# Kernel tuning notes

Hardware: AMD Instinct MI355X
Metric: run time of the kernel (lower is better)

The kernel has to match this reference:

```python
import jax, jax.numpy as jnp
import numpy as np

N = 100000      # nodes
IN = 64         # in_channels
HID = 64        # hidden_channels
H2 = HID // 2   # per-sign channels
E = 1600000     # edges per sign


def _mean_aggr(x_src, edge_index, num_nodes):
    """Mean of x_src[src] scattered onto dst (PyG mean aggregation)."""
    src, dst = edge_index[0], edge_index[1]
    s = jax.ops.segment_sum(x_src[src], dst, num_segments=num_nodes)
    cnt = jax.ops.segment_sum(jnp.ones((src.shape[0],), x_src.dtype), dst,
                              num_segments=num_nodes)
    return s / jnp.maximum(cnt, 1.0)[:, None]


def setup_inputs() -> dict:
    key = jax.random.key(0)
    ks = jax.random.split(key, 12)
    x = jax.random.normal(ks[0], (N, IN), jnp.float32)
    pos_edge_index = jax.random.randint(ks[1], (2, E), 0, N)
    neg_edge_index = jax.random.randint(ks[2], (2, E), 0, N)

    def w(k, fan_in, fan_out):
        b = 1.0 / np.sqrt(fan_in)
        return jax.random.uniform(k, (fan_in, fan_out), jnp.float32, -b, b)

    return dict(
        x=x, pos_edge_index=pos_edge_index, neg_edge_index=neg_edge_index,
        # conv1 (first_aggr=True): lin_l (no bias applied via l), lin_r (bias)
        w1_pl=w(ks[3], IN, H2), w1_pr=w(ks[4], IN, H2), b1_p=jnp.zeros((H2,), jnp.float32),
        w1_nl=w(ks[5], IN, H2), w1_nr=w(ks[6], IN, H2), b1_n=jnp.zeros((H2,), jnp.float32),
        # conv2 (first_aggr=False): lin_l over cat of two aggregations (2*H2), lin_r over H2
        w2_pl=w(ks[7], 2 * H2, H2), w2_pr=w(ks[8], H2, H2), b2_p=jnp.zeros((H2,), jnp.float32),
        w2_nl=w(ks[9], 2 * H2, H2), w2_nr=w(ks[10], H2, H2), b2_n=jnp.zeros((H2,), jnp.float32),
    )


def reference(x, pos_edge_index, neg_edge_index,
              w1_pl, w1_pr, b1_p, w1_nl, w1_nr, b1_n,
              w2_pl, w2_pr, b2_p, w2_nl, w2_nr, b2_n):
    n = x.shape[0]
    # --- conv1, first_aggr=True ---
    agg_p = _mean_aggr(x, pos_edge_index, n)          # [N, IN]
    agg_n = _mean_aggr(x, neg_edge_index, n)
    out_pos = agg_p @ w1_pl + x @ w1_pr + b1_p         # [N, H2]
    out_neg = agg_n @ w1_nl + x @ w1_nr + b1_n
    z = jax.nn.relu(jnp.concatenate([out_pos, out_neg], axis=-1))  # [N, HID]

    # --- conv2, first_aggr=False ---
    h2 = z.shape[-1] // 2
    zp, zn = z[:, :h2], z[:, h2:]
    p1 = _mean_aggr(zp, pos_edge_index, n)
    p2 = _mean_aggr(zn, neg_edge_index, n)
    out_pos = jnp.concatenate([p1, p2], axis=-1) @ w2_pl + zp @ w2_pr + b2_p
    n1 = _mean_aggr(zn, pos_edge_index, n)
    n2 = _mean_aggr(zp, neg_edge_index, n)
    out_neg = jnp.concatenate([n1, n2], axis=-1) @ w2_nl + zn @ w2_nr + b2_n
    z = jax.nn.relu(jnp.concatenate([out_pos, out_neg], axis=-1))  # [N, HID]
    return z
```

## Files before the change

kernel.cpp:

```cpp
#include <hip/hip_runtime.h>
#include <hip/hip_fp16.h>

using uint = unsigned int;

static constexpr int NN  = 100000;
static constexpr int NE  = 1600000;
static constexpr int DIM = 64;
static constexpr int HH  = 32;
static constexpr int NBLK = (NN + 255) / 256;
static constexpr int HB   = 256;
static constexpr int CHUNK = NE / HB;
static constexpr int BSH  = 9;
static constexpr int BSZ  = 512;
static constexpr int NBKT = (NN + BSZ - 1) / BSZ;

__device__ __forceinline__ float2 up16(uint v) {
  __half2 h = *reinterpret_cast<__half2*>(&v);
  return __half22float2(h);
}
__device__ __forceinline__ uint pk16(float a, float b) {
  __half2 h = __floats2half2_rn(a, b);
  return *reinterpret_cast<uint*>(&h);
}


__global__ void c_hist(const int* __restrict__ pe, const int* __restrict__ ne,
                       int* __restrict__ part_hist) {
  const int set = blockIdx.y;
  const int* dstA = (set ? ne : pe) + NE;
  __shared__ int h[256];
  h[threadIdx.x] = 0;
  __syncthreads();
  int lo = blockIdx.x * CHUNK;
  int hi = lo + CHUNK;
  for (int i = lo + threadIdx.x; i < hi; i += 256)
    atomicAdd(&h[dstA[i] >> BSH], 1);
  __syncthreads();
  part_hist[(set * HB + blockIdx.x) * 256 + threadIdx.x] = h[threadIdx.x];
}

__global__ void c_colscan(int* __restrict__ part_hist, int* __restrict__ tot) {
  const int set = blockIdx.y;
  const int k   = blockIdx.x;
  const int t   = threadIdx.x;
  int v = part_hist[(set * HB + t) * 256 + k];
  __shared__ int sm[256];
  sm[t] = v;
  __syncthreads();
  for (int off = 1; off < 256; off <<= 1) {
    int add = (t >= off) ? sm[t - off] : 0;
    __syncthreads();
    sm[t] += add;
    __syncthreads();
  }
  part_hist[(set * HB + t) * 256 + k] = (t == 0) ? 0 : sm[t - 1];
  if (t == 255) tot[set * 256 + k] = sm[255];
}

__global__ void c_basescan(const int* __restrict__ tot, int* __restrict__ base) {
  const int t   = threadIdx.x;
  const int seg = t >> 8;
  const int idx = t & 255;
  int v = tot[seg * 256 + idx];
  __shared__ int sm[512];
  sm[t] = v;
  __syncthreads();
  for (int off = 1; off < 256; off <<= 1) {
    int add = (idx >= off) ? sm[t - off] : 0;
    __syncthreads();
    sm[t] += add;
    __syncthreads();
  }
  base[seg * 257 + idx] = (idx == 0) ? 0 : sm[t - 1];
  if (idx == 255) base[seg * 257 + 256] = sm[t];
}

__global__ void c_scatter(const int* __restrict__ pe, const int* __restrict__ ne,
                          const int* __restrict__ part_hist, const int* __restrict__ base,
                          uint* __restrict__ partP, uint* __restrict__ partN) {
  const int set = blockIdx.y;
  const int* srcA = set ? ne : pe;
  const int* dstA = srcA + NE;
  uint* part = set ? partN : partP;
  __shared__ int off[256];
  off[threadIdx.x] = base[set * 257 + threadIdx.x] +
                     part_hist[(set * HB + blockIdx.x) * 256 + threadIdx.x];
  __syncthreads();
  int lo = blockIdx.x * CHUNK;
  int hi = lo + CHUNK;
  for (int i = lo + threadIdx.x; i < hi; i += 256) {
    int src = srcA[i];
    int dst = dstA[i];
    int pos = atomicAdd(&off[dst >> BSH], 1);
    part[pos] = ((uint)src << BSH) | (uint)(dst & (BSZ - 1));
  }
}

__global__ void c_bucket(const uint* __restrict__ partP, const uint* __restrict__ partN,
                         const int* __restrict__ base,
                         int* __restrict__ row_p, int* __restrict__ row_n,
                         int* __restrict__ col_p, int* __restrict__ col_n,
                         const float* __restrict__ x,
                         const float* __restrict__ w1_pl, const float* __restrict__ w1_pr,
                         const float* __restrict__ b1_p,
                         const float* __restrict__ w1_nl, const float* __restrict__ w1_nr,
                         const float* __restrict__ b1_n,
                         uint* __restrict__ y1u, float* __restrict__ r1) {
  const int bx = blockIdx.x;
  const int t  = threadIdx.x;

  if (bx < 2 * NBKT) {
    const int set = bx / NBKT;
    const int k   = bx - set * NBKT;
    const uint* part = set ? partN : partP;
    int* row = set ? row_n : row_p;
    int* col = set ? col_n : col_p;
    const int lo = k * BSZ;
    const int hi = min(lo + BSZ, NN);
    const int s = base[set * 257 + k];
    const int e = base[set * 257 + k + 1];

    __shared__ int cnt[BSZ], rowl[BSZ], cnt2[BSZ];
    cnt[t] = 0; cnt[t + 256] = 0;
    cnt2[t] = 0; cnt2[t + 256] = 0;
    __syncthreads();
    for (int i = s + t; i < e; i += 256)
      atomicAdd(&cnt[part[i] & (BSZ - 1)], 1);
    __syncthreads();
    rowl[t] = cnt[t]; rowl[t + 256] = cnt[t + 256];
    __syncthreads();
    for (int off = 1; off < BSZ; off <<= 1) {
      int a0 = (t >= off) ? rowl[t - off] : 0;
      int a1 = (t + 256 >= off) ? rowl[t + 256 - off] : 0;
      __syncthreads();
      rowl[t] += a0; rowl[t + 256] += a1;
      __syncthreads();
    }
    if (lo + t < hi)        row[lo + t]        = s + (t ? rowl[t - 1] : 0);
    if (lo + t + 256 < hi)  row[lo + t + 256]  = s + rowl[t + 255];
    if (k == NBKT - 1 && t == 0) row[NN] = NE;
    for (int i = s + t; i < e; i += 256) {
      uint p = part[i];
      int l = p & (BSZ - 1);
      int pos = s + (l ? rowl[l - 1] : 0) + atomicAdd(&cnt2[l], 1);
      col[pos] = (int)(p >> BSH);
    }
    return;
  }

  const int pb   = bx - 2 * NBKT;
  const int h    = (pb >= NBLK) ? 1 : 0;
  const int nblk = pb - (h ? NBLK : 0);
  const float* wl   = h ? w1_nl : w1_pl;
  const float* wr   = h ? w1_nr : w1_pr;
  const float* bias = h ? b1_n  : b1_p;

  __shared__ float s_wl[DIM][HH];
  __shared__ float s_wr[DIM][HH];
  for (int i = t; i < DIM * HH; i += 256) {
    s_wl[i >> 5][i & 31] = wl[i];
    s_wr[i >> 5][i & 31] = wr[i];
  }
  __syncthreads();

  int node = nblk * 256 + t;
  if (node >= NN) return;

  float ay[HH], ar[HH];
#pragma unroll
  for (int j = 0; j < HH; ++j) { ay[j] = 0.f; ar[j] = bias[j]; }

  const float4* xrow = (const float4*)(x + (size_t)node * DIM);
#pragma unroll 4
  for (int k4 = 0; k4 < DIM / 4; ++k4) {
    float4 xv = xrow[k4];
#pragma unroll
    for (int u = 0; u < 4; ++u) {
      int k = k4 * 4 + u;
      float xk = (&xv.x)[u];
#pragma unroll
      for (int j = 0; j < HH; ++j) {
        ay[j] += xk * s_wl[k][j];
        ar[j] += xk * s_wr[k][j];
      }
    }
  }

  uint*  yo = y1u + (size_t)node * 32 + h * 16;
  float* ro = r1  + (size_t)node * 64 + h * 32;
#pragma unroll
  for (int j = 0; j < 16; ++j) yo[j] = pk16(ay[2 * j], ay[2 * j + 1]);
#pragma unroll
  for (int j = 0; j < HH; ++j) ro[j] = ar[j];
}

__global__ void k_aggr1(const uint* __restrict__ y1u,
                        const int* __restrict__ rp, const int* __restrict__ cp,
                        const int* __restrict__ rn, const int* __restrict__ cn,
                        const float* r1,
                        float* z) {
  int gid  = blockIdx.x * 256 + threadIdx.x;
  int node = gid >> 6;
  if (node >= NN) return;
  int lane = threadIdx.x & 63;
  int g = lane >> 2;
  int f = lane & 3;

  int s = rp[node], e = rp[node + 1];
  float a[8];
#pragma unroll
  for (int j = 0; j < 8; ++j) a[j] = 0.f;
  for (int i = s + g; i < e; i += 16) {
    int c = cp[i];
    uint4 v = *(const uint4*)&y1u[(size_t)c * 32 + 4 * f];
    float2 p0 = up16(v.x), p1 = up16(v.y), p2 = up16(v.z), p3 = up16(v.w);
    a[0] += p0.x; a[1] += p0.y; a[2] += p1.x; a[3] += p1.y;
    a[4] += p2.x; a[5] += p2.y; a[6] += p3.x; a[7] += p3.y;
  }
#pragma unroll
  for (int w = 4; w <= 32; w <<= 1) {
#pragma unroll
    for (int j = 0; j < 8; ++j) a[j] += __shfl_xor(a[j], w);
  }
  float invp = 1.f / (float)max(e - s, 1);

  s = rn[node]; e = rn[node + 1];
  float b[8];
#pragma unroll
  for (int j = 0; j < 8; ++j) b[j] = 0.f;
  for (int i = s + g; i < e; i += 16) {
    int c = cn[i];
    uint4 v = *(const uint4*)&y1u[(size_t)c * 32 + 16 + 4 * f];
    float2 p0 = up16(v.x), p1 = up16(v.y), p2 = up16(v.z), p3 = up16(v.w);
    b[0] += p0.x; b[1] += p0.y; b[2] += p1.x; b[3] += p1.y;
    b[4] += p2.x; b[5] += p2.y; b[6] += p3.x; b[7] += p3.y;
  }
#pragma unroll
  for (int w = 4; w <= 32; w <<= 1) {
#pragma unroll
    for (int j = 0; j < 8; ++j) b[j] += __shfl_xor(b[j], w);
  }
  float invn = 1.f / (float)max(e - s, 1);

  size_t base = (size_t)node * 64;
  if (g == 0) {
    const float4 r0 = *(const float4*)(r1 + base + 8 * f);
    const float4 r1v = *(const float4*)(r1 + base + 8 * f + 4);
    float4 o0, o1;
    o0.x = fmaxf(a[0] * invp + r0.x, 0.f);
    o0.y = fmaxf(a[1] * invp + r0.y, 0.f);
    o0.z = fmaxf(a[2] * invp + r0.z, 0.f);
    o0.w = fmaxf(a[3] * invp + r0.w, 0.f);
    o1.x = fmaxf(a[4] * invp + r1v.x, 0.f);
    o1.y = fmaxf(a[5] * invp + r1v.y, 0.f);
    o1.z = fmaxf(a[6] * invp + r1v.z, 0.f);
    o1.w = fmaxf(a[7] * invp + r1v.w, 0.f);
    *(float4*)(z + base + 8 * f) = o0;
    *(float4*)(z + base + 8 * f + 4) = o1;
  } else if (g == 1) {
    const float4 r0 = *(const float4*)(r1 + base + 32 + 8 * f);
    const float4 r1v = *(const float4*)(r1 + base + 32 + 8 * f + 4);
    float4 o0, o1;
    o0.x = fmaxf(b[0] * invn + r0.x, 0.f);
    o0.y = fmaxf(b[1] * invn + r0.y, 0.f);
    o0.z = fmaxf(b[2] * invn + r0.z, 0.f);
    o0.w = fmaxf(b[3] * invn + r0.w, 0.f);
    o1.x = fmaxf(b[4] * invn + r1v.x, 0.f);
    o1.y = fmaxf(b[5] * invn + r1v.y, 0.f);
    o1.z = fmaxf(b[6] * invn + r1v.z, 0.f);
    o1.w = fmaxf(b[7] * invn + r1v.w, 0.f);
    *(float4*)(z + base + 32 + 8 * f) = o0;
    *(float4*)(z + base + 32 + 8 * f + 4) = o1;
  }
}

__global__ void k_mid(const float* __restrict__ z,
                      const float* __restrict__ w2_pl, const float* __restrict__ w2_pr,
                      const float* __restrict__ b2_p,
                      const float* __restrict__ w2_nl, const float* __restrict__ w2_nr,
                      const float* __restrict__ b2_n,
                      uint* __restrict__ u_pos, uint* __restrict__ u_neg,
                      float* __restrict__ r2) {
  const int t = blockIdx.y;
  const float* mat;
  const float* bias = nullptr;
  int srcHalf;
  switch (t) {
    case 0: mat = w2_pl;            srcHalf = 0; break;
    case 1: mat = w2_nl;            srcHalf = 1; break;
    case 2: mat = w2_pl + 32 * 32;  srcHalf = 1; break;
    case 3: mat = w2_nl + 32 * 32;  srcHalf = 0; break;
    case 4: mat = w2_pr; bias = b2_p; srcHalf = 0; break;
    default: mat = w2_nr; bias = b2_n; srcHalf = 1; break;
  }

  __shared__ float s_m[HH][HH];
  for (int i = threadIdx.x; i < HH * HH; i += 256) s_m[i >> 5][i & 31] = mat[i];
  __syncthreads();

  int node = blockIdx.x * 256 + threadIdx.x;
  if (node >= NN) return;

  float acc[HH];
#pragma unroll
  for (int j = 0; j < HH; ++j) acc[j] = bias ? bias[j] : 0.f;

  const float4* zrow = (const float4*)(z + (size_t)node * 64 + srcHalf * 32);
#pragma unroll 4
  for (int k4 = 0; k4 < HH / 4; ++k4) {
    float4 v = zrow[k4];
#pragma unroll
    for (int u = 0; u < 4; ++u) {
      int k = k4 * 4 + u;
      float vv = (&v.x)[u];
#pragma unroll
      for (int j = 0; j < HH; ++j) acc[j] += vv * s_m[k][j];
    }
  }

  if (t < 4) {
    uint* o = (t < 2 ? u_pos : u_neg) + (size_t)node * 32 + (t & 1) * 16;
#pragma unroll
    for (int j = 0; j < 16; ++j) o[j] = pk16(acc[2 * j], acc[2 * j + 1]);
  } else {
    float* o = r2 + (size_t)node * 64 + (t - 4) * 32;
#pragma unroll
    for (int j = 0; j < HH; ++j) o[j] = acc[j];
  }
}

__global__ void k_aggr2(const uint* __restrict__ u_pos, const uint* __restrict__ u_neg,
                        const int* __restrict__ rp, const int* __restrict__ cp,
                        const int* __restrict__ rn, const int* __restrict__ cn,
                        const float* __restrict__ r2,
                        float* __restrict__ out) {
  int gid  = blockIdx.x * 256 + threadIdx.x;
  int node = gid >> 6;
  if (node >= NN) return;
  int lane = threadIdx.x & 63;
  int g = lane >> 3;
  int f = lane & 7;

  int s = rp[node], e = rp[node + 1];
  float a[8];
#pragma unroll
  for (int j = 0; j < 8; ++j) a[j] = 0.f;
  for (int i = s + g; i < e; i += 8) {
    int c = cp[i];
    uint4 v = *(const uint4*)&u_pos[(size_t)c * 32 + 4 * f];
    float2 p0 = up16(v.x), p1 = up16(v.y), p2 = up16(v.z), p3 = up16(v.w);
    a[0] += p0.x; a[1] += p0.y; a[2] += p1.x; a[3] += p1.y;
    a[4] += p2.x; a[5] += p2.y; a[6] += p3.x; a[7] += p3.y;
  }
#pragma unroll
  for (int w = 8; w <= 32; w <<= 1) {
#pragma unroll
    for (int j = 0; j < 8; ++j) a[j] += __shfl_xor(a[j], w);
  }
  float invp = 1.f / (float)max(e - s, 1);

  s = rn[node]; e = rn[node + 1];
  float b[8];
#pragma unroll
  for (int j = 0; j < 8; ++j) b[j] = 0.f;
  for (int i = s + g; i < e; i += 8) {
    int c = cn[i];
    uint4 v = *(const uint4*)&u_neg[(size_t)c * 32 + 4 * f];
    float2 p0 = up16(v.x), p1 = up16(v.y), p2 = up16(v.z), p3 = up16(v.w);
    b[0] += p0.x; b[1] += p0.y; b[2] += p1.x; b[3] += p1.y;
    b[4] += p2.x; b[5] += p2.y; b[6] += p3.x; b[7] += p3.y;
  }
#pragma unroll
  for (int w = 8; w <= 32; w <<= 1) {
#pragma unroll
    for (int j = 0; j < 8; ++j) b[j] += __shfl_xor(b[j], w);
  }
  float invn = 1.f / (float)max(e - s, 1);

  if (g == 0) {
    size_t base = (size_t)node * 64 + 8 * f;
    const float4 r0 = *(const float4*)(r2 + base);
    const float4 r1v = *(const float4*)(r2 + base + 4);
    float4 o0, o1;
    o0.x = fmaxf(a[0] * invp + b[0] * invn + r0.x, 0.f);
    o0.y = fmaxf(a[1] * invp + b[1] * invn + r0.y, 0.f);
    o0.z = fmaxf(a[2] * invp + b[2] * invn + r0.z, 0.f);
    o0.w = fmaxf(a[3] * invp + b[3] * invn + r0.w, 0.f);
    o1.x = fmaxf(a[4] * invp + b[4] * invn + r1v.x, 0.f);
    o1.y = fmaxf(a[5] * invp + b[5] * invn + r1v.y, 0.f);
    o1.z = fmaxf(a[6] * invp + b[6] * invn + r1v.z, 0.f);
    o1.w = fmaxf(a[7] * invp + b[7] * invn + r1v.w, 0.f);
    *(float4*)(out + base) = o0;
    *(float4*)(out + base + 4) = o1;
  }
}


extern "C" void kernel_launch(void* const* d_in, const int* in_sizes, int n_in,
                              void* d_out, int out_size, void* d_ws, size_t ws_size,
                              hipStream_t stream) {
  const float* x     = (const float*)d_in[0];
  const int*   pe    = (const int*)d_in[1];
  const int*   ne    = (const int*)d_in[2];
  const float* w1_pl = (const float*)d_in[3];
  const float* w1_pr = (const float*)d_in[4];
  const float* b1_p  = (const float*)d_in[5];
  const float* w1_nl = (const float*)d_in[6];
  const float* w1_nr = (const float*)d_in[7];
  const float* b1_n  = (const float*)d_in[8];
  const float* w2_pl = (const float*)d_in[9];
  const float* w2_pr = (const float*)d_in[10];
  const float* b2_p  = (const float*)d_in[11];
  const float* w2_nl = (const float*)d_in[12];
  const float* w2_nr = (const float*)d_in[13];
  const float* b2_n  = (const float*)d_in[14];

  char* ws = (char*)d_ws;
  size_t off = 0;
  auto alloc = [&](size_t bytes) -> char* {
    char* p = ws + off;
    off = (off + bytes + 255) & ~(size_t)255;
    return p;
  };

  int* row_p = (int*)alloc((size_t)(NN + 1) * 4);
  int* row_n = (int*)alloc((size_t)(NN + 1) * 4);
  int* col_p = (int*)alloc((size_t)NE * 4);
  int* col_n = (int*)alloc((size_t)NE * 4);
  int* part_hist = (int*)alloc((size_t)2 * HB * 256 * 4);
  int* tot   = (int*)alloc((size_t)2 * 256 * 4);
  int* base  = (int*)alloc((size_t)2 * 257 * 4);

  char* regA  = alloc((size_t)NN * 64 * 4);
  uint* partP = (uint*)regA;
  uint* partN = (uint*)(regA + (size_t)NE * 4);
  uint* u_pos = (uint*)regA;
  uint* u_neg = (uint*)(regA + (size_t)NN * 32 * 4);

  char*  regB = alloc((size_t)NN * 64 * 4);
  uint*  y1u  = (uint*)regB;
  float* r2   = (float*)regB;

  float* r1 = (float*)d_out;
  float* z  = (float*)d_out;

  const int nb = NBLK;
  const int ab = (NN * 64 + 255) / 256;

  dim3 hg(HB, 2);
  c_hist<<<hg, 256, 0, stream>>>(pe, ne, part_hist);
  dim3 cg(256, 2);
  c_colscan<<<cg, 256, 0, stream>>>(part_hist, tot);
  c_basescan<<<1, 512, 0, stream>>>(tot, base);
  c_scatter<<<hg, 256, 0, stream>>>(pe, ne, part_hist, base, partP, partN);
  c_bucket<<<2 * NBKT + 2 * NBLK, 256, 0, stream>>>(
      partP, partN, base, row_p, row_n, col_p, col_n,
      x, w1_pl, w1_pr, b1_p, w1_nl, w1_nr, b1_n, y1u, r1);

  k_aggr1<<<ab, 256, 0, stream>>>(y1u, row_p, col_p, row_n, col_n, r1, z);

  dim3 g2(nb, 6);
  k_mid<<<g2, 256, 0, stream>>>(z, w2_pl, w2_pr, b2_p, w2_nl, w2_nr, b2_n,
                                u_pos, u_neg, r2);

  k_aggr2<<<ab, 256, 0, stream>>>(u_pos, u_neg, row_p, col_p, row_n, col_n, r2,
                                  (float*)d_out);
}
```

Baseline: 287.3 us.

## Halve CSR bucket size, fuse layer-1 GEMM into scatter kernel, split y1 per sign

Coarse buckets shrink from 512 to 256 nodes, so there are 512 coarse buckets with matching histogram, scan and base arrays. The dense layer-1 projection moves out of the bucket kernel and into the coarse-scatter launch, so it runs alongside the edge scatter instead of the fine bucketing. The half-precision y1 buffer is also split into separate positive and negative arrays of 16 uints per node, which makes each gather read from a compact array. The risks are more shared-memory atomics contention per coarse bucket and a larger base scan, which now uses a 1024-thread block.

```diff
diff --git a/kernel.cpp b/kernel.cpp
--- a/kernel.cpp
+++ b/kernel.cpp
@@ -10,8 +10,8 @@
 static constexpr int NBLK = (NN + 255) / 256;
 static constexpr int HB   = 256;
 static constexpr int CHUNK = NE / HB;
-static constexpr int BSH  = 9;
-static constexpr int BSZ  = 512;
+static constexpr int BSH  = 8;
+static constexpr int BSZ  = 256;
 static constexpr int NBKT = (NN + BSZ - 1) / BSZ;
 
 __device__ __forceinline__ float2 up16(uint v) {
@@ -28,22 +28,24 @@
                        int* __restrict__ part_hist) {
   const int set = blockIdx.y;
   const int* dstA = (set ? ne : pe) + NE;
-  __shared__ int h[256];
-  h[threadIdx.x] = 0;
+  __shared__ int h[512];
+  h[threadIdx.x] = 0; h[threadIdx.x + 256] = 0;
   __syncthreads();
   int lo = blockIdx.x * CHUNK;
   int hi = lo + CHUNK;
   for (int i = lo + threadIdx.x; i < hi; i += 256)
     atomicAdd(&h[dstA[i] >> BSH], 1);
   __syncthreads();
-  part_hist[(set * HB + blockIdx.x) * 256 + threadIdx.x] = h[threadIdx.x];
+  int* o = part_hist + (size_t)(set * HB + blockIdx.x) * 512;
+  o[threadIdx.x] = h[threadIdx.x];
+  o[threadIdx.x + 256] = h[threadIdx.x + 256];
 }
 
 __global__ void c_colscan(int* __restrict__ part_hist, int* __restrict__ tot) {
   const int set = blockIdx.y;
   const int k   = blockIdx.x;
   const int t   = threadIdx.x;
-  int v = part_hist[(set * HB + t) * 256 + k];
+  int v = part_hist[(size_t)(set * HB + t) * 512 + k];
   __shared__ int sm[256];
   sm[t] = v;
   __syncthreads();
@@ -53,113 +55,76 @@
     sm[t] += add;
     __syncthreads();
   }
-  part_hist[(set * HB + t) * 256 + k] = (t == 0) ? 0 : sm[t - 1];
-  if (t == 255) tot[set * 256 + k] = sm[255];
+  part_hist[(size_t)(set * HB + t) * 512 + k] = (t == 0) ? 0 : sm[t - 1];
+  if (t == 255) tot[set * 512 + k] = sm[255];
 }
 
 __global__ void c_basescan(const int* __restrict__ tot, int* __restrict__ base) {
   const int t   = threadIdx.x;
-  const int seg = t >> 8;
-  const int idx = t & 255;
-  int v = tot[seg * 256 + idx];
-  __shared__ int sm[512];
+  const int seg = t >> 9;
+  const int idx = t & 511;
+  int v = tot[seg * 512 + idx];
+  __shared__ int sm[1024];
   sm[t] = v;
   __syncthreads();
-  for (int off = 1; off < 256; off <<= 1) {
+  for (int off = 1; off < 512; off <<= 1) {
     int add = (idx >= off) ? sm[t - off] : 0;
     __syncthreads();
     sm[t] += add;
     __syncthreads();
   }
-  base[seg * 257 + idx] = (idx == 0) ? 0 : sm[t - 1];
-  if (idx == 255) base[seg * 257 + 256] = sm[t];
-}
-
-__global__ void c_scatter(const int* __restrict__ pe, const int* __restrict__ ne,
+  base[seg * 513 + idx] = (idx == 0) ? 0 : sm[t - 1];
+  if (idx == 511) base[seg * 513 + 512] = sm[t];
+}
+
+__global__ void c_scatpre(const int* __restrict__ pe, const int* __restrict__ ne,
                           const int* __restrict__ part_hist, const int* __restrict__ base,
-                          uint* __restrict__ partP, uint* __restrict__ partN) {
-  const int set = blockIdx.y;
-  const int* srcA = set ? ne : pe;
-  const int* dstA = srcA + NE;
-  uint* part = set ? partN : partP;
-  __shared__ int off[256];
-  off[threadIdx.x] = base[set * 257 + threadIdx.x] +
-                     part_hist[(set * HB + blockIdx.x) * 256 + threadIdx.x];
-  __syncthreads();
-  int lo = blockIdx.x * CHUNK;
-  int hi = lo + CHUNK;
-  for (int i = lo + threadIdx.x; i < hi; i += 256) {
-    int src = srcA[i];
-    int dst = dstA[i];
-    int pos = atomicAdd(&off[dst >> BSH], 1);
-    part[pos] = ((uint)src << BSH) | (uint)(dst & (BSZ - 1));
-  }
-}
-
-__global__ void c_bucket(const uint* __restrict__ partP, const uint* __restrict__ partN,
-                         const int* __restrict__ base,
-                         int* __restrict__ row_p, int* __restrict__ row_n,
-                         int* __restrict__ col_p, int* __restrict__ col_n,
-                         const float* __restrict__ x,
-                         const float* __restrict__ w1_pl, const float* __restrict__ w1_pr,
-                         const float* __restrict__ b1_p,
-                         const float* __restrict__ w1_nl, const float* __restrict__ w1_nr,
-                         const float* __restrict__ b1_n,
-                         uint* __restrict__ y1u, float* __restrict__ r1) {
+                          uint* __restrict__ partP, uint* __restrict__ partN,
+                          const float* __restrict__ x,
+                          const float* __restrict__ w1_pl, const float* __restrict__ w1_pr,
+                          const float* __restrict__ b1_p,
+                          const float* __restrict__ w1_nl, const float* __restrict__ w1_nr,
+                          const float* __restrict__ b1_n,
+                          uint* __restrict__ y1p, uint* __restrict__ y1n,
+                          float* __restrict__ r1) {
+  __shared__ uint smem[4096];
   const int bx = blockIdx.x;
   const int t  = threadIdx.x;
 
-  if (bx < 2 * NBKT) {
-    const int set = bx / NBKT;
-    const int k   = bx - set * NBKT;
-    const uint* part = set ? partN : partP;
-    int* row = set ? row_n : row_p;
-    int* col = set ? col_n : col_p;
-    const int lo = k * BSZ;
-    const int hi = min(lo + BSZ, NN);
-    const int s = base[set * 257 + k];
-    const int e = base[set * 257 + k + 1];
-
-    __shared__ int cnt[BSZ], rowl[BSZ], cnt2[BSZ];
-    cnt[t] = 0; cnt[t + 256] = 0;
-    cnt2[t] = 0; cnt2[t + 256] = 0;
-    __syncthreads();
-    for (int i = s + t; i < e; i += 256)
-      atomicAdd(&cnt[part[i] & (BSZ - 1)], 1);
-    __syncthreads();
-    rowl[t] = cnt[t]; rowl[t + 256] = cnt[t + 256];
-    __syncthreads();
-    for (int off = 1; off < BSZ; off <<= 1) {
-      int a0 = (t >= off) ? rowl[t - off] : 0;
-      int a1 = (t + 256 >= off) ? rowl[t + 256 - off] : 0;
-      __syncthreads();
-      rowl[t] += a0; rowl[t + 256] += a1;
-      __syncthreads();
-    }
-    if (lo + t < hi)        row[lo + t]        = s + (t ? rowl[t - 1] : 0);
-    if (lo + t + 256 < hi)  row[lo + t + 256]  = s + rowl[t + 255];
-    if (k == NBKT - 1 && t == 0) row[NN] = NE;
-    for (int i = s + t; i < e; i += 256) {
-      uint p = part[i];
-      int l = p & (BSZ - 1);
-      int pos = s + (l ? rowl[l - 1] : 0) + atomicAdd(&cnt2[l], 1);
-      col[pos] = (int)(p >> BSH);
+  if (bx < 512) {
+    const int set = bx >> 8;
+    const int b   = bx & 255;
+    const int* srcA = set ? ne : pe;
+    const int* dstA = srcA + NE;
+    uint* part = set ? partN : partP;
+    int* off = (int*)smem;
+    const int* ph = part_hist + (size_t)(set * HB + b) * 512;
+    off[t]       = base[set * 513 + t]       + ph[t];
+    off[t + 256] = base[set * 513 + t + 256] + ph[t + 256];
+    __syncthreads();
+    int lo = b * CHUNK;
+    int hi = lo + CHUNK;
+    for (int i = lo + t; i < hi; i += 256) {
+      int src = srcA[i];
+      int dst = dstA[i];
+      int pos = atomicAdd(&off[dst >> BSH], 1);
+      part[pos] = ((uint)src << BSH) | (uint)(dst & (BSZ - 1));
     }
     return;
   }
 
-  const int pb   = bx - 2 * NBKT;
+  const int pb   = bx - 512;
   const int h    = (pb >= NBLK) ? 1 : 0;
   const int nblk = pb - (h ? NBLK : 0);
   const float* wl   = h ? w1_nl : w1_pl;
   const float* wr   = h ? w1_nr : w1_pr;
   const float* bias = h ? b1_n  : b1_p;
 
-  __shared__ float s_wl[DIM][HH];
-  __shared__ float s_wr[DIM][HH];
+  float* s_wl = (float*)smem;
+  float* s_wr = (float*)smem + 2048;
   for (int i = t; i < DIM * HH; i += 256) {
-    s_wl[i >> 5][i & 31] = wl[i];
-    s_wr[i >> 5][i & 31] = wr[i];
+    s_wl[i] = wl[i];
+    s_wr[i] = wr[i];
   }
   __syncthreads();
 
@@ -180,21 +145,61 @@
       float xk = (&xv.x)[u];
 #pragma unroll
       for (int j = 0; j < HH; ++j) {
-        ay[j] += xk * s_wl[k][j];
-        ar[j] += xk * s_wr[k][j];
+        ay[j] += xk * s_wl[k * HH + j];
+        ar[j] += xk * s_wr[k * HH + j];
       }
     }
   }
 
-  uint*  yo = y1u + (size_t)node * 32 + h * 16;
-  float* ro = r1  + (size_t)node * 64 + h * 32;
+  uint*  yo = (h ? y1n : y1p) + (size_t)node * 16;
+  float* ro = r1 + (size_t)node * 64 + h * 32;
 #pragma unroll
   for (int j = 0; j < 16; ++j) yo[j] = pk16(ay[2 * j], ay[2 * j + 1]);
 #pragma unroll
   for (int j = 0; j < HH; ++j) ro[j] = ar[j];
 }
 
-__global__ void k_aggr1(const uint* __restrict__ y1u,
+__global__ void c_bucket(const uint* __restrict__ partP, const uint* __restrict__ partN,
+                         const int* __restrict__ base,
+                         int* __restrict__ row_p, int* __restrict__ row_n,
+                         int* __restrict__ col_p, int* __restrict__ col_n) {
+  const int bx = blockIdx.x;
+  const int t  = threadIdx.x;
+  const int set = (bx >= NBKT) ? 1 : 0;
+  const int k   = bx - (set ? NBKT : 0);
+  const uint* part = set ? partN : partP;
+  int* row = set ? row_n : row_p;
+  int* col = set ? col_n : col_p;
+  const int lo = k * BSZ;
+  const int hi = min(lo + BSZ, NN);
+  const int s = base[set * 513 + k];
+  const int e = base[set * 513 + k + 1];
+
+  __shared__ int cnt[BSZ], rowl[BSZ], cnt2[BSZ];
+  cnt[t] = 0; cnt2[t] = 0;
+  __syncthreads();
+  for (int i = s + t; i < e; i += 256)
+    atomicAdd(&cnt[part[i] & (BSZ - 1)], 1);
+  __syncthreads();
+  rowl[t] = cnt[t];
+  __syncthreads();
+  for (int off = 1; off < BSZ; off <<= 1) {
+    int a0 = (t >= off) ? rowl[t - off] : 0;
+    __syncthreads();
+    rowl[t] += a0;
+    __syncthreads();
+  }
+  if (lo + t < hi) row[lo + t] = s + (t ? rowl[t - 1] : 0);
+  if (k == NBKT - 1 && t == 0) row[NN] = NE;
+  for (int i = s + t; i < e; i += 256) {
+    uint p = part[i];
+    int l = p & (BSZ - 1);
+    int pos = s + (l ? rowl[l - 1] : 0) + atomicAdd(&cnt2[l], 1);
+    col[pos] = (int)(p >> BSH);
+  }
+}
+
+__global__ void k_aggr1(const uint* __restrict__ y1p, const uint* __restrict__ y1n,
                         const int* __restrict__ rp, const int* __restrict__ cp,
                         const int* __restrict__ rn, const int* __restrict__ cn,
                         const float* r1,
@@ -212,7 +217,7 @@
   for (int j = 0; j < 8; ++j) a[j] = 0.f;
   for (int i = s + g; i < e; i += 16) {
     int c = cp[i];
-    uint4 v = *(const uint4*)&y1u[(size_t)c * 32 + 4 * f];
+    uint4 v = *(const uint4*)&y1p[(size_t)c * 16 + 4 * f];
     float2 p0 = up16(v.x), p1 = up16(v.y), p2 = up16(v.z), p3 = up16(v.w);
     a[0] += p0.x; a[1] += p0.y; a[2] += p1.x; a[3] += p1.y;
     a[4] += p2.x; a[5] += p2.y; a[6] += p3.x; a[7] += p3.y;
@@ -230,7 +235,7 @@
   for (int j = 0; j < 8; ++j) b[j] = 0.f;
   for (int i = s + g; i < e; i += 16) {
     int c = cn[i];
-    uint4 v = *(const uint4*)&y1u[(size_t)c * 32 + 16 + 4 * f];
+    uint4 v = *(const uint4*)&y1n[(size_t)c * 16 + 4 * f];
     float2 p0 = up16(v.x), p1 = up16(v.y), p2 = up16(v.z), p3 = up16(v.w);
     b[0] += p0.x; b[1] += p0.y; b[2] += p1.x; b[3] += p1.y;
     b[4] += p2.x; b[5] += p2.y; b[6] += p3.x; b[7] += p3.y;
@@ -427,9 +432,9 @@
   int* row_n = (int*)alloc((size_t)(NN + 1) * 4);
   int* col_p = (int*)alloc((size_t)NE * 4);
   int* col_n = (int*)alloc((size_t)NE * 4);
-  int* part_hist = (int*)alloc((size_t)2 * HB * 256 * 4);
-  int* tot   = (int*)alloc((size_t)2 * 256 * 4);
-  int* base  = (int*)alloc((size_t)2 * 257 * 4);
+  int* part_hist = (int*)alloc((size_t)2 * HB * 512 * 4);
+  int* tot   = (int*)alloc((size_t)2 * 512 * 4);
+  int* base  = (int*)alloc((size_t)2 * 513 * 4);
 
   char* regA  = alloc((size_t)NN * 64 * 4);
   uint* partP = (uint*)regA;
@@ -438,7 +443,8 @@
   uint* u_neg = (uint*)(regA + (size_t)NN * 32 * 4);
 
   char*  regB = alloc((size_t)NN * 64 * 4);
-  uint*  y1u  = (uint*)regB;
+  uint*  y1p  = (uint*)regB;
+  uint*  y1n  = (uint*)(regB + (size_t)NN * 16 * 4);
   float* r2   = (float*)regB;
 
   float* r1 = (float*)d_out;
@@ -449,15 +455,16 @@
 
   dim3 hg(HB, 2);
   c_hist<<<hg, 256, 0, stream>>>(pe, ne, part_hist);
-  dim3 cg(256, 2);
+  dim3 cg(512, 2);
   c_colscan<<<cg, 256, 0, stream>>>(part_hist, tot);
-  c_basescan<<<1, 512, 0, stream>>>(tot, base);
-  c_scatter<<<hg, 256, 0, stream>>>(pe, ne, part_hist, base, partP, partN);
-  c_bucket<<<2 * NBKT + 2 * NBLK, 256, 0, stream>>>(
-      partP, partN, base, row_p, row_n, col_p, col_n,
-      x, w1_pl, w1_pr, b1_p, w1_nl, w1_nr, b1_n, y1u, r1);
-
-  k_aggr1<<<ab, 256, 0, stream>>>(y1u, row_p, col_p, row_n, col_n, r1, z);
+  c_basescan<<<1, 1024, 0, stream>>>(tot, base);
+  c_scatpre<<<512 + 2 * NBLK, 256, 0, stream>>>(
+      pe, ne, part_hist, base, partP, partN,
+      x, w1_pl, w1_pr, b1_p, w1_nl, w1_nr, b1_n, y1p, y1n, r1);
+  c_bucket<<<2 * NBKT, 256, 0, stream>>>(partP, partN, base,
+                                         row_p, row_n, col_p, col_n);
+
+  k_aggr1<<<ab, 256, 0, stream>>>(y1p, y1n, row_p, col_p, row_n, col_n, r1, z);
 
   dim3 g2(nb, 6);
   k_mid<<<g2, 256, 0, stream>>>(z, w2_pl, w2_pr, b2_p, w2_nl, w2_nr, b2_n,
```

After: 304.0 us. 5.8% more time.
